# Performance work log

Measured on AMD Instinct MI355X. Metric: run time of the kernel, lower is better.

The kernel has to match this reference:

```python
import jax, jax.numpy as jnp
import numpy as np

B, D, M, R, C = 1024, 32, 8, 4096, 32
TOPK_P = 0.1  # hard-coded in torch forward
EPS = 1e-9


def setup_inputs() -> dict:
    key = jax.random.key(0)
    k0, k1, k2, k3, k4 = jax.random.split(key, 5)
    x = jax.random.normal(k0, (B, D), dtype=jnp.float32)
    centers = jax.random.normal(k1, (D, M), dtype=jnp.float32)
    # widths kept away from 0 so gaussian MFs don't all underflow
    widths = jax.random.uniform(k2, (D, M), dtype=jnp.float32, minval=0.5, maxval=1.5)
    consequents = jax.random.uniform(k3, (R, D + 1, C), dtype=jnp.float32)
    rules = jax.random.randint(k4, (R, D), 0, M, dtype=jnp.int32)
    return {"x": x, "centers": centers, "widths": widths,
            "consequents": consequents, "rules": rules}


def reference(x, centers, widths, consequents, rules):
    Bn, Dn = x.shape
    Rn = rules.shape[0]
    # Gaussian membership functions: (B, D, M)
    mfs = jnp.exp(-((x[:, :, None] - centers[None]) ** 2) / (2.0 * widths[None] ** 2))
    # Gather per-rule MF values: (B, D, R)  (torch.gather along mf axis)
    rule_mfs = mfs[:, jnp.arange(Dn)[:, None], rules.T]
    # Firing strengths via product over input dims: (B, R)
    firing = jnp.prod(rule_mfs, axis=1)
    # top-K gate + scatter mask
    K = max(1, int(TOPK_P * Rn))
    _, idx = jax.lax.top_k(firing, K)
    mask = jnp.zeros_like(firing).at[jnp.arange(Bn)[:, None], idx].set(1.0)
    firing = firing * mask
    norm_fs = firing / (firing.sum(axis=1, keepdims=True) + EPS)
    # zeroG=False branch. Torch does einsum('bi,rjc->brc', x_ext, consequents)
    # which sums i and j independently: rule_mfs[b,r,c] = sum_i(x_ext[b,i]) * sum_j(cons[r,j,c]).
    # Then einsum('br,brc->bc') => out = sum(x_ext,1) * (norm_fs @ sum(cons,1)).
    x_ext_sum = x.sum(axis=1) + 1.0          # sum over x_ext = [x, 1], shape (B,)
    cons_sum = consequents.sum(axis=1)       # (R, C)
    rule_outputs = x_ext_sum[:, None] * (norm_fs @ cons_sum)  # (B, C)
    return rule_outputs, norm_fs, mask
```

## Files before the change

kernel.cpp:

```cpp
#include <hip/hip_runtime.h>

#define Bn 1024
#define Dn 32
#define Mn 8
#define Rn 4096
#define Cn 32
#define Kn 409
#define NTH 256
#define RPT 16
#define NBIN 2048
#define CCAP 256

typedef unsigned long long u64;
typedef unsigned int u32;

__device__ __forceinline__ int binof(float kf) {
    int b = (int)floorf(kf * (float)(NBIN / 120.0) + (float)NBIN);
    b = b < 0 ? 0 : b;
    b = b > (NBIN - 1) ? (NBIN - 1) : b;
    return b;
}

__device__ __forceinline__ double rule_sum(const uint4 q, const double* __restrict__ e2) {
    double s = 0.0;
#define LK(w, j, pb) e2[(((pb) + (j)) << 6) + (((w) >> (8 * (j))) & 63u)]
    s += LK(q.x, 0, 0);  s += LK(q.x, 1, 0);  s += LK(q.x, 2, 0);  s += LK(q.x, 3, 0);
    s += LK(q.y, 0, 4);  s += LK(q.y, 1, 4);  s += LK(q.y, 2, 4);  s += LK(q.y, 3, 4);
    s += LK(q.z, 0, 8);  s += LK(q.z, 1, 8);  s += LK(q.z, 2, 8);  s += LK(q.z, 3, 8);
    s += LK(q.w, 0, 12); s += LK(q.w, 1, 12); s += LK(q.w, 2, 12); s += LK(q.w, 3, 12);
#undef LK
    return s;
}

__global__ __launch_bounds__(256) void pack_rules_kernel(const int* __restrict__ rules,
                                                         uint4* __restrict__ packed) {
    int r = blockIdx.x * 256 + threadIdx.x;
    if (r >= Rn) return;
    const int* rp = rules + r * Dn;
    u32 w[4];
#pragma unroll
    for (int wi = 0; wi < 4; ++wi) {
        u32 v = 0;
#pragma unroll
        for (int j = 0; j < 4; ++j) {
            int p = wi * 4 + j;
            u32 m0 = (u32)rp[2 * p] & 7u;
            u32 m1 = (u32)rp[2 * p + 1] & 7u;
            v |= (m0 | (m1 << 3)) << (8 * j);
        }
        w[wi] = v;
    }
    packed[r] = make_uint4(w[0], w[1], w[2], w[3]);
}

__global__ __launch_bounds__(256) void cons_sum_kernel(const float* __restrict__ cons,
                                                       float* __restrict__ out) {
    int idx = blockIdx.x * 256 + threadIdx.x;
    if (idx >= Rn * Cn) return;
    int r = idx >> 5;
    int c = idx & 31;
    const float* p = cons + (size_t)r * (Dn + 1) * Cn + c;
    float s = 0.0f;
#pragma unroll
    for (int k = 0; k < Dn + 1; ++k) s += p[(size_t)k * Cn];
    out[idx] = s;
}

#define OFF_SCAN 8192
#define OFF_CIDX 0
#define OFF_CVAL 1024
#define OFF_CFLG 3072
#define OFF_SIDX 4096
#define OFF_SVAL 5760
#define OFF_RED  7424

__global__ __launch_bounds__(NTH, 4) void anfis_kernel(
    const float* __restrict__ x,
    const float* __restrict__ centers,
    const float* __restrict__ widths,
    const uint4* __restrict__ rpack,
    const float* __restrict__ cons_sum,
    float* __restrict__ out_rule,
    float* __restrict__ out_norm,
    float* __restrict__ out_mask)
{
    __shared__ float s_key[Rn];
    __shared__ double s_e2[16 * 64];
    __shared__ __align__(16) char s_buf[9216];
    __shared__ float s_x[Dn];
    __shared__ int s_bb, s_nab, s_ccnt, s_scnt;
    __shared__ float s_denomf;

    const int t = threadIdx.x;
    const int b = blockIdx.x;

    if (t < Dn) s_x[t] = x[b * Dn + t];
    if (t == 0) { s_ccnt = 0; s_scnt = 0; s_denomf = 0.0f; }
    __syncthreads();

    double* s_e = (double*)s_buf;
    {
        const int d = t >> 3;
        double dx = (double)s_x[d] - (double)centers[t];
        double w = (double)widths[t];
        s_e[t] = -(dx * dx) / (2.0 * (w * w));
    }
    __syncthreads();

    for (int k = t; k < 16 * 64; k += NTH) {
        int p = k >> 6, c = k & 63;
        s_e2[k] = s_e[(2 * p) * 8 + (c & 7)] + s_e[(2 * p + 1) * 8 + (c >> 3)];
    }
    __syncthreads();

    u32* s_hist = (u32*)s_buf;
    for (int k = t; k < NBIN; k += NTH) s_hist[k] = 0u;
#pragma unroll
    for (int i = 0; i < RPT; ++i) {
        const int r = i * NTH + t;
        s_key[r] = (float)rule_sum(rpack[r], s_e2);
    }
    __syncthreads();

#pragma unroll
    for (int i = 0; i < RPT; ++i) {
        const int r = i * NTH + t;
        atomicAdd(&s_hist[binof(s_key[r])], 1u);
    }
    __syncthreads();

    int* s_scan = (int*)(s_buf + OFF_SCAN);
    const int base = t * 8;
    int loc = 0;
#pragma unroll
    for (int j = 0; j < 8; ++j) loc += (int)s_hist[base + j];
    int v = loc;
    s_scan[t] = v;
    __syncthreads();
#pragma unroll
    for (int off = 1; off < 256; off <<= 1) {
        int a = (t + off < 256) ? s_scan[t + off] : 0;
        __syncthreads();
        v += a;
        s_scan[t] = v;
        __syncthreads();
    }
    const int excl = v - loc;
    if (excl < Kn && v >= Kn) {
        int c = excl;
        for (int j = 7; j >= 0; --j) {
            int h = (int)s_hist[base + j];
            if (c < Kn && c + h >= Kn) { s_bb = base + j; s_nab = c; }
            c += h;
        }
    }
    __syncthreads();
    const int bb = s_bb;
    const int n_above = s_nab;
    const int want_bin = Kn - n_above;
    __syncthreads();

    int* s_cidx = (int*)(s_buf + OFF_CIDX);
    double* s_cval = (double*)(s_buf + OFF_CVAL);
    int* s_cflag = (int*)(s_buf + OFF_CFLG);
#pragma unroll
    for (int i = 0; i < RPT; ++i) {
        const int r = i * NTH + t;
        if (binof(s_key[r]) == bb) {
            int pos = atomicAdd(&s_ccnt, 1);
            if (pos < CCAP) {
                s_cidx[pos] = r;
                s_cval[pos] = rule_sum(rpack[r], s_e2);
            }
        }
    }
    __syncthreads();
    const int cnt = (s_ccnt < CCAP) ? s_ccnt : CCAP;
    if (t < cnt) {
        const double mv = s_cval[t];
        const int mi = s_cidx[t];
        int rank = 0;
        for (int j = 0; j < cnt; ++j) {
            double ov = s_cval[j];
            int oi = s_cidx[j];
            rank += ((ov > mv) || (ov == mv && oi < mi)) ? 1 : 0;
        }
        s_cflag[t] = (rank < want_bin) ? 1 : 0;
    }
    __syncthreads();

    u32 selbits = 0u;
    float lsum = 0.0f;
#pragma unroll
    for (int i = 0; i < RPT; ++i) {
        const int r = i * NTH + t;
        const float kf = s_key[r];
        const int bin = binof(kf);
        bool sel = (bin > bb);
        if (bin == bb) {
            for (int j = 0; j < cnt; ++j) {
                if (s_cidx[j] == r) { sel = (s_cflag[j] != 0); break; }
            }
        }
        if (sel) { selbits |= (1u << i); lsum += __expf(0.0f) * 0.0f + expf(kf); }
    }
#pragma unroll
    for (int off = 32; off >= 1; off >>= 1) lsum += __shfl_xor(lsum, off);
    if ((t & 63) == 0) atomicAdd(&s_denomf, lsum);
    __syncthreads();
    const float denom = s_denomf + 1e-9f;

    int* s_selidx = (int*)(s_buf + OFF_SIDX);
    float* s_selv = (float*)(s_buf + OFF_SVAL);
    float* onorm = out_norm + (size_t)b * Rn;
    float* omask = out_mask + (size_t)b * Rn;
#pragma unroll
    for (int i = 0; i < RPT; ++i) {
        const int r = i * NTH + t;
        const bool sel = (selbits >> i) & 1u;
        float nv = 0.0f;
        if (sel) {
            nv = expf(s_key[r]) / denom;
            int p = atomicAdd(&s_scnt, 1);
            s_selidx[p] = r;
            s_selv[p] = nv;
        }
        onorm[r] = nv;
        omask[r] = sel ? 1.0f : 0.0f;
    }
    __syncthreads();

    const int nsel = s_scnt;
    const int g = t >> 5;
    const int c = t & 31;
    float acc = 0.0f;
    for (int i = g; i < nsel; i += 8) {
        acc += s_selv[i] * cons_sum[s_selidx[i] * Cn + c];
    }
    float* s_red = (float*)(s_buf + OFF_RED);
    s_red[t] = acc;
    __syncthreads();
    if (t < Cn) {
        float ss = 0.0f;
#pragma unroll
        for (int gg = 0; gg < 8; ++gg) ss += s_red[gg * 32 + t];
        float xs = 1.0f;
#pragma unroll
        for (int d = 0; d < Dn; ++d) xs += s_x[d];
        out_rule[b * Cn + t] = xs * ss;
    }
}

extern "C" void kernel_launch(void* const* d_in, const int* in_sizes, int n_in,
                              void* d_out, int out_size, void* d_ws, size_t ws_size,
                              hipStream_t stream) {
    (void)in_sizes; (void)n_in; (void)out_size; (void)ws_size;
    const float* x = (const float*)d_in[0];
    const float* centers = (const float*)d_in[1];
    const float* widths = (const float*)d_in[2];
    const float* consequents = (const float*)d_in[3];
    const int* rules = (const int*)d_in[4];

    float* out_rule = (float*)d_out;
    float* out_norm = out_rule + (size_t)Bn * Cn;
    float* out_mask = out_norm + (size_t)Bn * Rn;

    float* cons_sum = (float*)d_ws;
    uint4* rpack = (uint4*)((char*)d_ws + (size_t)Rn * Cn * sizeof(float));

    pack_rules_kernel<<<Rn / 256, 256, 0, stream>>>(rules, rpack);
    cons_sum_kernel<<<(Rn * Cn) / 256, 256, 0, stream>>>(consequents, cons_sum);
    anfis_kernel<<<Bn, 256, 0, stream>>>(x, centers, widths, rpack, cons_sum,
                                         out_rule, out_norm, out_mask);
}
```

Measured before the change: 52.31 us.

## Rework ANFIS top-k kernel: 512 threads, register keys, fp32 lookup, wave scans

Doubles the block to 512 threads and halves rules per thread. Firing keys now stay in registers instead of a 16 KB shared array. The pairwise log-MF lookup table is stored in float rather than double, and boundary-bin candidates are recomputed exactly in double from the per-dim table. The 8-pass block-wide histogram scan is replaced by wave shuffles, and the atomic compaction of selected rules by a deterministic prefix-sum. These changes aim to cut shared memory, barriers and atomics to raise occupancy, at the cost of fp32 key rounding near bin edges and more registers per thread.

```diff
diff --git a/kernel.cpp b/kernel.cpp
--- a/kernel.cpp
+++ b/kernel.cpp
@@ -6,29 +6,37 @@
 #define Rn 4096
 #define Cn 32
 #define Kn 409
-#define NTH 256
-#define RPT 16
-#define NBIN 2048
+#define NTH 512
+#define RPT 8
+#define NBIN 1024
 #define CCAP 256
 
-typedef unsigned long long u64;
 typedef unsigned int u32;
 
 __device__ __forceinline__ int binof(float kf) {
     int b = (int)floorf(kf * (float)(NBIN / 120.0) + (float)NBIN);
-    b = b < 0 ? 0 : b;
-    b = b > (NBIN - 1) ? (NBIN - 1) : b;
-    return b;
-}
-
-__device__ __forceinline__ double rule_sum(const uint4 q, const double* __restrict__ e2) {
+    return b < 0 ? 0 : (b > NBIN - 1 ? NBIN - 1 : b);
+}
+
+__device__ __forceinline__ float rule_sum_f32(const uint4 q, const float* __restrict__ e2) {
+    float s = 0.f;
+    const u32 wv[4] = {q.x, q.y, q.z, q.w};
+#pragma unroll
+    for (int p = 0; p < 16; ++p) {
+        s += e2[(p << 6) + ((wv[p >> 2] >> (8 * (p & 3))) & 63u)];
+    }
+    return s;
+}
+
+__device__ __forceinline__ double rule_sum_f64(const uint4 q, const double* __restrict__ e) {
     double s = 0.0;
-#define LK(w, j, pb) e2[(((pb) + (j)) << 6) + (((w) >> (8 * (j))) & 63u)]
-    s += LK(q.x, 0, 0);  s += LK(q.x, 1, 0);  s += LK(q.x, 2, 0);  s += LK(q.x, 3, 0);
-    s += LK(q.y, 0, 4);  s += LK(q.y, 1, 4);  s += LK(q.y, 2, 4);  s += LK(q.y, 3, 4);
-    s += LK(q.z, 0, 8);  s += LK(q.z, 1, 8);  s += LK(q.z, 2, 8);  s += LK(q.z, 3, 8);
-    s += LK(q.w, 0, 12); s += LK(q.w, 1, 12); s += LK(q.w, 2, 12); s += LK(q.w, 3, 12);
-#undef LK
+    const u32 wv[4] = {q.x, q.y, q.z, q.w};
+#pragma unroll
+    for (int p = 0; p < 16; ++p) {
+        const u32 byte = (wv[p >> 2] >> (8 * (p & 3))) & 63u;
+        s += e[(2 * p) * 8 + (byte & 7u)];
+        s += e[(2 * p + 1) * 8 + (byte >> 3)];
+    }
     return s;
 }
 
@@ -66,15 +74,7 @@
     out[idx] = s;
 }
 
-#define OFF_SCAN 8192
-#define OFF_CIDX 0
-#define OFF_CVAL 1024
-#define OFF_CFLG 3072
-#define OFF_SIDX 4096
-#define OFF_SVAL 5760
-#define OFF_RED  7424
-
-__global__ __launch_bounds__(NTH, 4) void anfis_kernel(
+__global__ __launch_bounds__(NTH, 8) void anfis_kernel(
     const float* __restrict__ x,
     const float* __restrict__ centers,
     const float* __restrict__ widths,
@@ -84,98 +84,97 @@
     float* __restrict__ out_norm,
     float* __restrict__ out_mask)
 {
-    __shared__ float s_key[Rn];
-    __shared__ double s_e2[16 * 64];
-    __shared__ __align__(16) char s_buf[9216];
-    __shared__ float s_x[Dn];
-    __shared__ int s_bb, s_nab, s_ccnt, s_scnt;
-    __shared__ float s_denomf;
+    __shared__ float  s_e2[16 * 64];
+    __shared__ double s_e[Dn * Mn];
+    __shared__ u32    s_hist[NBIN];
+    __shared__ int    s_wtot[8];
+    __shared__ float  s_wsum[8];
+    __shared__ int    s_cidx[CCAP];
+    __shared__ double s_cval[CCAP];
+    __shared__ int    s_cflag[CCAP];
+    __shared__ int    s_selidx[Kn + 8];
+    __shared__ float  s_selv[Kn + 8];
+    __shared__ float  s_red[NTH];
+    __shared__ float  s_x[Dn];
+    __shared__ int    s_bb, s_nab, s_ccnt;
 
     const int t = threadIdx.x;
+    const int lane = t & 63;
+    const int w = t >> 6;
     const int b = blockIdx.x;
 
     if (t < Dn) s_x[t] = x[b * Dn + t];
-    if (t == 0) { s_ccnt = 0; s_scnt = 0; s_denomf = 0.0f; }
-    __syncthreads();
-
-    double* s_e = (double*)s_buf;
-    {
+    if (t == 0) s_ccnt = 0;
+    __syncthreads();
+
+    if (t < Dn * Mn) {
         const int d = t >> 3;
         double dx = (double)s_x[d] - (double)centers[t];
-        double w = (double)widths[t];
-        s_e[t] = -(dx * dx) / (2.0 * (w * w));
-    }
-    __syncthreads();
-
+        double ww = (double)widths[t];
+        s_e[t] = -(dx * dx) / (2.0 * (ww * ww));
+    }
+    __syncthreads();
+
+#pragma unroll
     for (int k = t; k < 16 * 64; k += NTH) {
         int p = k >> 6, c = k & 63;
-        s_e2[k] = s_e[(2 * p) * 8 + (c & 7)] + s_e[(2 * p + 1) * 8 + (c >> 3)];
-    }
-    __syncthreads();
-
-    u32* s_hist = (u32*)s_buf;
-    for (int k = t; k < NBIN; k += NTH) s_hist[k] = 0u;
+        s_e2[k] = (float)(s_e[(2 * p) * 8 + (c & 7)] + s_e[(2 * p + 1) * 8 + (c >> 3)]);
+    }
+    s_hist[t] = 0u;
+    s_hist[t + NTH] = 0u;
+    __syncthreads();
+
+    float kf[RPT];
 #pragma unroll
     for (int i = 0; i < RPT; ++i) {
         const int r = i * NTH + t;
-        s_key[r] = (float)rule_sum(rpack[r], s_e2);
-    }
-    __syncthreads();
-
-#pragma unroll
-    for (int i = 0; i < RPT; ++i) {
-        const int r = i * NTH + t;
-        atomicAdd(&s_hist[binof(s_key[r])], 1u);
-    }
-    __syncthreads();
-
-    int* s_scan = (int*)(s_buf + OFF_SCAN);
-    const int base = t * 8;
-    int loc = 0;
-#pragma unroll
-    for (int j = 0; j < 8; ++j) loc += (int)s_hist[base + j];
-    int v = loc;
-    s_scan[t] = v;
-    __syncthreads();
-#pragma unroll
-    for (int off = 1; off < 256; off <<= 1) {
-        int a = (t + off < 256) ? s_scan[t + off] : 0;
-        __syncthreads();
-        v += a;
-        s_scan[t] = v;
-        __syncthreads();
-    }
-    const int excl = v - loc;
-    if (excl < Kn && v >= Kn) {
-        int c = excl;
-        for (int j = 7; j >= 0; --j) {
-            int h = (int)s_hist[base + j];
-            if (c < Kn && c + h >= Kn) { s_bb = base + j; s_nab = c; }
-            c += h;
+        const float s = rule_sum_f32(rpack[r], s_e2);
+        kf[i] = s;
+        atomicAdd(&s_hist[binof(s)], 1u);
+    }
+    __syncthreads();
+
+    const int h0 = (int)s_hist[2 * t];
+    const int h1 = (int)s_hist[2 * t + 1];
+    const int loc = h0 + h1;
+    int S = loc;
+#pragma unroll
+    for (int off = 1; off < 64; off <<= 1) {
+        int vv = __shfl(S, lane + off < 64 ? lane + off : lane);
+        if (lane + off < 64) S += vv;
+    }
+    if (lane == 0) s_wtot[w] = S;
+    __syncthreads();
+    int wsuf = 0;
+#pragma unroll
+    for (int ww = 0; ww < 8; ++ww) wsuf += (ww > w) ? s_wtot[ww] : 0;
+    {
+        const int excl = (S - loc) + wsuf;
+        const int vtot = excl + loc;
+        if (excl < Kn && vtot >= Kn) {
+            int c = excl;
+            if (c < Kn && c + h1 >= Kn) { s_bb = 2 * t + 1; s_nab = c; }
+            c += h1;
+            if (c < Kn && c + h0 >= Kn) { s_bb = 2 * t; s_nab = c; }
         }
     }
     __syncthreads();
     const int bb = s_bb;
-    const int n_above = s_nab;
-    const int want_bin = Kn - n_above;
-    __syncthreads();
-
-    int* s_cidx = (int*)(s_buf + OFF_CIDX);
-    double* s_cval = (double*)(s_buf + OFF_CVAL);
-    int* s_cflag = (int*)(s_buf + OFF_CFLG);
-#pragma unroll
-    for (int i = 0; i < RPT; ++i) {
-        const int r = i * NTH + t;
-        if (binof(s_key[r]) == bb) {
+    const int want_bin = Kn - s_nab;
+
+#pragma unroll
+    for (int i = 0; i < RPT; ++i) {
+        if (binof(kf[i]) == bb) {
+            const int r = i * NTH + t;
             int pos = atomicAdd(&s_ccnt, 1);
             if (pos < CCAP) {
                 s_cidx[pos] = r;
-                s_cval[pos] = rule_sum(rpack[r], s_e2);
+                s_cval[pos] = rule_sum_f64(rpack[r], s_e);
             }
         }
     }
     __syncthreads();
-    const int cnt = (s_ccnt < CCAP) ? s_ccnt : CCAP;
+    const int cnt = s_ccnt < CCAP ? s_ccnt : CCAP;
     if (t < cnt) {
         const double mv = s_cval[t];
         const int mi = s_cidx[t];
@@ -190,61 +189,73 @@
     __syncthreads();
 
     u32 selbits = 0u;
-    float lsum = 0.0f;
+    int cnt_sel = 0;
+    float lsum = 0.f;
 #pragma unroll
     for (int i = 0; i < RPT; ++i) {
         const int r = i * NTH + t;
-        const float kf = s_key[r];
-        const int bin = binof(kf);
+        const int bin = binof(kf[i]);
         bool sel = (bin > bb);
         if (bin == bb) {
+            sel = false;
             for (int j = 0; j < cnt; ++j) {
                 if (s_cidx[j] == r) { sel = (s_cflag[j] != 0); break; }
             }
         }
-        if (sel) { selbits |= (1u << i); lsum += __expf(0.0f) * 0.0f + expf(kf); }
+        float f = 0.f;
+        if (sel) { f = expf(kf[i]); selbits |= (1u << i); ++cnt_sel; lsum += f; }
+        kf[i] = f;
     }
 #pragma unroll
     for (int off = 32; off >= 1; off >>= 1) lsum += __shfl_xor(lsum, off);
-    if ((t & 63) == 0) atomicAdd(&s_denomf, lsum);
-    __syncthreads();
-    const float denom = s_denomf + 1e-9f;
-
-    int* s_selidx = (int*)(s_buf + OFF_SIDX);
-    float* s_selv = (float*)(s_buf + OFF_SVAL);
+    if (lane == 0) s_wsum[w] = lsum;
+    int p = cnt_sel;
+#pragma unroll
+    for (int off = 1; off < 64; off <<= 1) {
+        int u = __shfl(p, lane >= off ? lane - off : lane);
+        if (lane >= off) p += u;
+    }
+    if (lane == 63) s_wtot[w] = p;
+    __syncthreads();
+    float denom = 1e-9f;
+#pragma unroll
+    for (int ww = 0; ww < 8; ++ww) denom += s_wsum[ww];
+    int base = 0;
+#pragma unroll
+    for (int ww = 0; ww < 8; ++ww) base += (ww < w) ? s_wtot[ww] : 0;
+    int pos = base + (p - cnt_sel);
+
     float* onorm = out_norm + (size_t)b * Rn;
     float* omask = out_mask + (size_t)b * Rn;
 #pragma unroll
     for (int i = 0; i < RPT; ++i) {
         const int r = i * NTH + t;
         const bool sel = (selbits >> i) & 1u;
-        float nv = 0.0f;
+        float nv = 0.f;
         if (sel) {
-            nv = expf(s_key[r]) / denom;
-            int p = atomicAdd(&s_scnt, 1);
-            s_selidx[p] = r;
-            s_selv[p] = nv;
+            nv = kf[i] / denom;
+            s_selidx[pos] = r;
+            s_selv[pos] = nv;
+            ++pos;
         }
         onorm[r] = nv;
-        omask[r] = sel ? 1.0f : 0.0f;
-    }
-    __syncthreads();
-
-    const int nsel = s_scnt;
+        omask[r] = sel ? 1.f : 0.f;
+    }
+    __syncthreads();
+
     const int g = t >> 5;
     const int c = t & 31;
-    float acc = 0.0f;
-    for (int i = g; i < nsel; i += 8) {
+    float acc = 0.f;
+    for (int i = g; i < Kn; i += 16) {
         acc += s_selv[i] * cons_sum[s_selidx[i] * Cn + c];
     }
-    float* s_red = (float*)(s_buf + OFF_RED);
     s_red[t] = acc;
     __syncthreads();
     if (t < Cn) {
-        float ss = 0.0f;
-#pragma unroll
-        for (int gg = 0; gg < 8; ++gg) ss += s_red[gg * 32 + t];
-        float xs = 1.0f;
+        float ss = 0.f;
+#pragma unroll
+        for (int gg = 0; gg < 16; ++gg) ss += s_red[gg * 32 + t];
+        float xs = 1.f;
 #pragma unroll
         for (int d = 0; d < Dn; ++d) xs += s_x[d];
         out_rule[b * Cn + t] = xs * ss;
@@ -270,6 +281,6 @@
 
     pack_rules_kernel<<<Rn / 256, 256, 0, stream>>>(rules, rpack);
     cons_sum_kernel<<<(Rn * Cn) / 256, 256, 0, stream>>>(consequents, cons_sum);
-    anfis_kernel<<<Bn, 256, 0, stream>>>(x, centers, widths, rpack, cons_sum,
+    anfis_kernel<<<Bn, NTH, 0, stream>>>(x, centers, widths, rpack, cons_sum,
                                          out_rule, out_norm, out_mask);
 }
```

After: 50.67 us. 3.1% less time.
